# Optimization experiments

Measured on AMD Instinct MI355X. Metric: run time of the kernel, lower is better.

## Reference

```python
import jax, jax.numpy as jnp
import numpy as np

HEADS = 4


def setup_inputs() -> dict:
    key = jax.random.key(0)
    ks = jax.random.split(key, 6)
    b, c, d, h, w = 4, 512, 16, 16, 16
    x = jax.random.normal(ks[0], (b, c, d, h, w), dtype=jnp.float32)
    s = 0.02  # param init scale
    Wq = jax.random.normal(ks[1], (c, c), dtype=jnp.float32) * s
    Wk = jax.random.normal(ks[2], (c, c), dtype=jnp.float32) * s
    Wv = jax.random.normal(ks[3], (c, c), dtype=jnp.float32) * s
    Wproj = jax.random.normal(ks[4], (c, c), dtype=jnp.float32) * s
    bproj = jnp.zeros((c,), dtype=jnp.float32)
    return {"x": x, "Wq": Wq, "Wk": Wk, "Wv": Wv, "Wproj": Wproj, "bproj": bproj}


def reference(x, Wq, Wk, Wv, Wproj, bproj):
    b, c, d, h, w = x.shape
    N = d * h * w
    scale = (c // HEADS) ** -0.5  # module uses ch//heads for scale
    xf = x.reshape(b, c, N)  # (b, c, N)
    # 1x1 Conv1d == channel matmul
    q = jnp.einsum('oc,bcn->bon', Wq, xf)
    k = jnp.einsum('oc,bcn->bon', Wk, xf)
    v = jnp.einsum('oc,bcn->bon', Wv, xf)
    # Faithful to original (buggy) view: split SEQUENCE dim by heads -> (b, H, c, N//H)
    q = q.reshape(b, HEADS, c, N // HEADS)
    k = k.reshape(b, HEADS, c, N // HEADS)
    v = v.reshape(b, HEADS, c, N // HEADS)
    attn = jax.nn.softmax(jnp.einsum('bhqe,bhke->bhqk', q, k) * scale, axis=-1)
    out = jnp.einsum('bhqk,bhke->bhqe', attn, v)  # (b, H, c, N//H)
    out = jnp.swapaxes(out, 2, 3).reshape(b, c, N)  # matches transpose(2,3).view
    out = jnp.einsum('oc,bcn->bon', Wproj, out) + bproj[None, :, None]
    return out.reshape(b, c, d, h, w) + x
```

## Files before the change

### kernel.cpp

```cpp
#include <hip/hip_runtime.h>
#include <stdint.h>


typedef __attribute__((ext_vector_type(8))) short short8;
typedef __attribute__((ext_vector_type(4))) float f32x4;

typedef const __attribute__((address_space(1))) unsigned int* gas_ptr;
typedef __attribute__((address_space(3))) unsigned int* las_ptr;

#define ATTN_SCALE 0.08838834764831845f

__device__ __forceinline__ unsigned short f2bf(float f) {
    union { float f; unsigned int u; } c; c.f = f;
    unsigned int u = c.u;
    u += 0x7fffu + ((u >> 16) & 1u);
    return (unsigned short)(u >> 16);
}

__device__ __forceinline__ void gl_lds16(const void* g, void* l) {
    __builtin_amdgcn_global_load_lds((gas_ptr)(uintptr_t)g, (las_ptr)(uintptr_t)l,
                                     16, 0, 0);
}

template<int LDA, int LDB, int KDIM, bool PERMB = false>
__device__ __forceinline__ void mfma_core(
    const unsigned short* __restrict__ A,
    const unsigned short* __restrict__ B,
    int m0, int n0,
    unsigned short* __restrict__ sA, unsigned short* __restrict__ sB,
    f32x4 acc[4][4])
{
    const int tid  = threadIdx.x;
    const int lane = tid & 63, wave = tid >> 6;
    const int lr = lane >> 2, lc = lane & 3;
    const int wm = (wave & 1) * 64, wn = (wave >> 1) * 64;
    const int col = lane & 15, quad = lane >> 4;

    const unsigned short* ga = A + (size_t)(m0 + 32 * wave + lr) * LDA + lc * 8;
    int rb0 = n0 + 32 * wave + lr;
    int rb1 = rb0 + 16;
    if (PERMB) {
        rb0 = 4 * (rb0 & 127) + (rb0 >> 7);
        rb1 = 4 * (rb1 & 127) + (rb1 >> 7);
    }
    const unsigned short* gb0 = B + (size_t)rb0 * LDB + lc * 8;
    const unsigned short* gb1 = B + (size_t)rb1 * LDB + lc * 8;

    unsigned short* la0 = sA + (32 * wave) * 32;
    unsigned short* la1 = sA + (32 * wave + 16) * 32;
    unsigned short* lb0 = sB + (32 * wave) * 32;
    unsigned short* lb1 = sB + (32 * wave + 16) * 32;

    for (int k0 = 0; k0 < KDIM; k0 += 32) {
        gl_lds16(ga + k0,            la0);
        gl_lds16(ga + k0 + 16 * LDA, la1);
        gl_lds16(gb0 + k0,           lb0);
        gl_lds16(gb1 + k0,           lb1);
        __syncthreads();
        short8 af[4], bf[4];
        #pragma unroll
        for (int i = 0; i < 4; ++i)
            af[i] = *(const short8*)&sA[(wm + i * 16 + col) * 32 + quad * 8];
        #pragma unroll
        for (int j = 0; j < 4; ++j)
            bf[j] = *(const short8*)&sB[(wn + j * 16 + col) * 32 + quad * 8];
        #pragma unroll
        for (int i = 0; i < 4; ++i)
            #pragma unroll
            for (int j = 0; j < 4; ++j)
                acc[i][j] = __builtin_amdgcn_mfma_f32_16x16x32_bf16(
                    af[i], bf[j], acc[i][j], 0, 0, 0);
        __syncthreads();
    }
}

__global__ __launch_bounds__(256)
void prep(const float* __restrict__ x,
          const float* __restrict__ Wq, const float* __restrict__ Wk,
          const float* __restrict__ Wv, const float* __restrict__ Wp,
          unsigned short* __restrict__ xT, unsigned short* __restrict__ Wb)
{
    if (blockIdx.z == 4) {
        const int idx = (blockIdx.y * 64 + blockIdx.x) * 256 + threadIdx.x;
        const int mat = idx >> 16;
        const int off = (idx & 65535) << 2;
        const float* src = (mat == 0 ? Wq : mat == 1 ? Wk : mat == 2 ? Wv : Wp) + off;
        const float4 f = *(const float4*)src;
        uint2 o;
        o.x = f2bf(f.x) | ((unsigned)f2bf(f.y) << 16);
        o.y = f2bf(f.z) | ((unsigned)f2bf(f.w) << 16);
        *(uint2*)&Wb[mat * 262144 + off] = o;
        return;
    }
    const int b = blockIdx.z;
    const int l = threadIdx.x & 63, w = threadIdx.x >> 6;
    const int n  = blockIdx.x * 64 + l;
    const int c0 = blockIdx.y * 32 + w * 8;
    const float* xp = x + (size_t)b * 2097152 + (size_t)c0 * 4096 + n;
    unsigned int p[4];
    #pragma unroll
    for (int j = 0; j < 4; ++j) {
        const unsigned short a  = f2bf(xp[(2 * j)     * 4096]);
        const unsigned short bb = f2bf(xp[(2 * j + 1) * 4096]);
        p[j] = a | ((unsigned)bb << 16);
    }
    uint4 v; v.x = p[0]; v.y = p[1]; v.z = p[2]; v.w = p[3];
    *(uint4*)&xT[(size_t)b * 2097152 + (size_t)n * 512 + c0] = v;
}

__global__ __launch_bounds__(256)
void gemm_qkv(const unsigned short* __restrict__ Wb,
              const unsigned short* __restrict__ xT,
              unsigned short* __restrict__ qb, unsigned short* __restrict__ kb,
              unsigned short* __restrict__ vT)
{
    __shared__ unsigned short sA[128 * 32], sB[128 * 32];

    const int z = blockIdx.z, wsel = z >> 2, b = z & 3;
    const unsigned short* A = Wb + wsel * 262144;
    const unsigned short* B = xT + (size_t)b * 2097152;
    const int m0 = blockIdx.y * 128, n0 = blockIdx.x * 128;

    f32x4 z4 = {0.f, 0.f, 0.f, 0.f};
    f32x4 acc[4][4];
    #pragma unroll
    for (int i = 0; i < 4; ++i)
        #pragma unroll
        for (int j = 0; j < 4; ++j) acc[i][j] = z4;

    mfma_core<512, 512, 512>(A, B, m0, n0, sA, sB, acc);

    const int lane = threadIdx.x & 63, wave = threadIdx.x >> 6;
    const int wm = (wave & 1) * 64, wn = (wave >> 1) * 64;
    const int col = lane & 15, quad = lane >> 4;

    if (wsel < 2) {
        unsigned short* C = (wsel == 0 ? qb : kb) + (size_t)b * 2097152;
        #pragma unroll
        for (int i = 0; i < 4; ++i)
            #pragma unroll
            for (int r = 0; r < 4; ++r) {
                const int row = m0 + wm + i * 16 + quad * 4 + r;
                #pragma unroll
                for (int j = 0; j < 4; ++j)
                    C[(size_t)row * 4096 + n0 + wn + j * 16 + col] = f2bf(acc[i][j][r]);
            }
    } else {
        const int h = m0 >> 7, s = n0 >> 10, e0 = n0 & 1023;
        unsigned short* dst = vT + (size_t)(b * 4 + h) * 524288 + s * 128;
        #pragma unroll
        for (int i = 0; i < 4; ++i) {
            const int kb2 = wm + i * 16 + quad * 4;
            #pragma unroll
            for (int j = 0; j < 4; ++j) {
                const int e = e0 + wn + j * 16 + col;
                uint2 o;
                o.x = f2bf(acc[i][j][0]) | ((unsigned)f2bf(acc[i][j][1]) << 16);
                o.y = f2bf(acc[i][j][2]) | ((unsigned)f2bf(acc[i][j][3]) << 16);
                *(uint2*)&dst[(size_t)e * 512 + kb2] = o;
            }
        }
    }
}

__global__ __launch_bounds__(256)
void gemm_qk(const unsigned short* __restrict__ qb,
             const unsigned short* __restrict__ kb,
             float* __restrict__ S)
{
    __shared__ unsigned short sA[128 * 32], sB[128 * 32];
    const int z = blockIdx.z;
    const int slab = z >> 1, half = z & 1;
    const unsigned short* A = qb + (size_t)slab * 524288 + half * 512;
    const unsigned short* B = kb + (size_t)slab * 524288 + half * 512;
    float* Sp = S + (size_t)half * 4194304 + (size_t)slab * 262144;
    const int m0 = blockIdx.y * 128, n0 = blockIdx.x * 128;

    f32x4 z4 = {0.f, 0.f, 0.f, 0.f};
    f32x4 acc[4][4];
    #pragma unroll
    for (int i = 0; i < 4; ++i)
        #pragma unroll
        for (int j = 0; j < 4; ++j) acc[i][j] = z4;

    mfma_core<1024, 1024, 512, true>(A, B, m0, n0, sA, sB, acc);

    const int lane = threadIdx.x & 63, wave = threadIdx.x >> 6;
    const int wm = (wave & 1) * 64, wn = (wave >> 1) * 64;
    const int col = lane & 15, quad = lane >> 4;
    #pragma unroll
    for (int i = 0; i < 4; ++i)
        #pragma unroll
        for (int r = 0; r < 4; ++r) {
            const int row = m0 + wm + i * 16 + quad * 4 + r;
            #pragma unroll
            for (int j = 0; j < 4; ++j)
                Sp[(size_t)row * 512 + n0 + wn + j * 16 + col] =
                    acc[i][j][r] * ATTN_SCALE;
        }
}

__global__ __launch_bounds__(256)
void softmax_rows(const float* __restrict__ S, unsigned short* __restrict__ P)
{
    const int wave = threadIdx.x >> 6, lane = threadIdx.x & 63;
    const int row  = blockIdx.x * 4 + wave;
    const float* p0 = S + (size_t)row * 512;
    const float* p1 = p0 + 4194304;
    unsigned short* o = P + (size_t)row * 512;

    float vals[8];
    float m = -1e30f;
    #pragma unroll
    for (int t = 0; t < 8; ++t) {
        vals[t] = p0[lane + t * 64] + p1[lane + t * 64];
        m = fmaxf(m, vals[t]);
    }
    #pragma unroll
    for (int s = 32; s > 0; s >>= 1) m = fmaxf(m, __shfl_xor(m, s));
    float sum = 0.f;
    #pragma unroll
    for (int t = 0; t < 8; ++t) { vals[t] = __expf(vals[t] - m); sum += vals[t]; }
    #pragma unroll
    for (int s = 32; s > 0; s >>= 1) sum += __shfl_xor(sum, s);
    const float inv = 1.f / sum;
    #pragma unroll
    for (int t = 0; t < 8; ++t) o[lane + t * 64] = f2bf(vals[t] * inv);
}

__global__ __launch_bounds__(256)
void gemm_pv(const unsigned short* __restrict__ Pb,
             const unsigned short* __restrict__ vT,
             unsigned short* __restrict__ yT)
{
    __shared__ unsigned short sT[128 * 136];
    unsigned short* sA = sT;
    unsigned short* sB = sT + 4096;
    const int z = blockIdx.z, b = z >> 2, hh = z & 3;
    const unsigned short* A = Pb + (size_t)z * 262144;
    const unsigned short* B = vT + (size_t)z * 524288;
    unsigned short* yTb = yT + (size_t)b * 2097152;
    const int m0 = blockIdx.y * 128;
    const int n0 = blockIdx.x * 128;

    f32x4 z4 = {0.f, 0.f, 0.f, 0.f};
    f32x4 acc[4][4];
    #pragma unroll
    for (int i = 0; i < 4; ++i)
        #pragma unroll
        for (int j = 0; j < 4; ++j) acc[i][j] = z4;

    mfma_core<512, 512, 512>(A, B, m0, n0, sA, sB, acc);

    const int tid = threadIdx.x;
    const int lane = tid & 63, wave = tid >> 6;
    const int wm = (wave & 1) * 64, wn = (wave >> 1) * 64;
    const int col = lane & 15, quad = lane >> 4;

    #pragma unroll
    for (int i = 0; i < 4; ++i)
        #pragma unroll
        for (int r = 0; r < 4; ++r) {
            const int rr = wm + i * 16 + quad * 4 + r;
            #pragma unroll
            for (int j = 0; j < 4; ++j)
                sT[rr * 136 + wn + j * 16 + col] = f2bf(acc[i][j][r]);
        }
    __syncthreads();

    #pragma unroll
    for (int k = 0; k < 4; ++k) {
        const int rid = k * 256 + tid;
        const int qq_l = rid >> 3, s = rid & 7;
        const unsigned short* Trow = sT + qq_l * 136;
        unsigned int p[8];
        #pragma unroll
        for (int t = 0; t < 8; ++t) {
            const unsigned int a  = Trow[s + 8 * (2 * t)];
            const unsigned int bb = Trow[s + 8 * (2 * t + 1)];
            p[t] = a | (bb << 16);
        }
        const size_t base = (size_t)((s << 9) + m0 + qq_l) * 512 + hh * 128 + (n0 >> 3);
        uint4 lo; lo.x = p[0]; lo.y = p[1]; lo.z = p[2]; lo.w = p[3];
        uint4 hi; hi.x = p[4]; hi.y = p[5]; hi.z = p[6]; hi.w = p[7];
        *(uint4*)&yTb[base]     = lo;
        *(uint4*)&yTb[base + 8] = hi;
    }
}

__global__ __launch_bounds__(256)
void gemm_proj(const unsigned short* __restrict__ Wpb,
               const unsigned short* __restrict__ yT,
               const float* __restrict__ bias, const float* __restrict__ x,
               float* __restrict__ out)
{
    __shared__ unsigned short sA[128 * 32], sB[128 * 32];
    const int b = blockIdx.z;
    const unsigned short* B = yT + (size_t)b * 2097152;
    const int m0 = blockIdx.y * 128, n0 = blockIdx.x * 128;

    f32x4 z4 = {0.f, 0.f, 0.f, 0.f};
    f32x4 acc[4][4];
    #pragma unroll
    for (int i = 0; i < 4; ++i)
        #pragma unroll
        for (int j = 0; j < 4; ++j) acc[i][j] = z4;

    mfma_core<512, 512, 512>(Wpb, B, m0, n0, sA, sB, acc);

    const int lane = threadIdx.x & 63, wave = threadIdx.x >> 6;
    const int wm = (wave & 1) * 64, wn = (wave >> 1) * 64;
    const int col = lane & 15, quad = lane >> 4;
    const size_t boff = (size_t)b * 2097152;
    #pragma unroll
    for (int i = 0; i < 4; ++i)
        #pragma unroll
        for (int r = 0; r < 4; ++r) {
            const int row = m0 + wm + i * 16 + quad * 4 + r;
            const float bi = bias[row];
            #pragma unroll
            for (int j = 0; j < 4; ++j) {
                const size_t idx = boff + (size_t)row * 4096 + n0 + wn + j * 16 + col;
                out[idx] = acc[i][j][r] + bi + x[idx];
            }
        }
}

extern "C" void kernel_launch(void* const* d_in, const int* in_sizes, int n_in,
                              void* d_out, int out_size, void* d_ws, size_t ws_size,
                              hipStream_t stream) {
    const float* x     = (const float*)d_in[0];
    const float* Wq    = (const float*)d_in[1];
    const float* Wk    = (const float*)d_in[2];
    const float* Wv    = (const float*)d_in[3];
    const float* Wproj = (const float*)d_in[4];
    const float* bproj = (const float*)d_in[5];
    float* out = (float*)d_out;

    char* w = (char*)d_ws;
    unsigned short* xT = (unsigned short*)(w + 0);
    unsigned short* qb = (unsigned short*)(w + 16777216);
    unsigned short* kb = (unsigned short*)(w + 33554432);
    unsigned short* vT = (unsigned short*)(w + 50331648);
    float*          S  = (float*)        (w + 67108864);
    unsigned short* Pb = (unsigned short*)(w + 100663296);
    unsigned short* Wb = (unsigned short*)(w + 109051904);
    unsigned short* yT = xT;

    prep        <<<dim3(64, 16, 5),  256, 0, stream>>>(x, Wq, Wk, Wv, Wproj, xT, Wb);
    gemm_qkv    <<<dim3(32, 4, 12),  256, 0, stream>>>(Wb, xT, qb, kb, vT);
    gemm_qk     <<<dim3(4, 4, 32),   256, 0, stream>>>(qb, kb, S);
    softmax_rows<<<dim3(2048),       256, 0, stream>>>(S, Pb);
    gemm_pv     <<<dim3(8, 4, 16),   256, 0, stream>>>(Pb, vT, yT);
    gemm_proj   <<<dim3(32, 4, 4),   256, 0, stream>>>(Wb + 3 * 262144, yT, bproj, x, out);
}
```

Measured before the change: 206.1 us.

## Double-buffer LDS tiles in shared MFMA GEMM core and swizzle LDS layout

```diff
diff --git a/kernel.cpp b/kernel.cpp
--- a/kernel.cpp
+++ b/kernel.cpp
@@ -33,44 +33,65 @@
     const int tid  = threadIdx.x;
     const int lane = tid & 63, wave = tid >> 6;
     const int lr = lane >> 2, lc = lane & 3;
-    const int wm = (wave & 1) * 64, wn = (wave >> 1) * 64;
-    const int col = lane & 15, quad = lane >> 4;
-
-    const unsigned short* ga = A + (size_t)(m0 + 32 * wave + lr) * LDA + lc * 8;
+    const int lcs = lc ^ ((lr >> 1) & 3);
+    const int wm = (wave & 1) * 64, wn = (wave >> 1) * 64;
+    const int col = lane & 15, quad = lane >> 4;
+    const int swz = (quad ^ ((col >> 1) & 3)) * 8;
+
+    const unsigned short* ga = A + (size_t)(m0 + 32 * wave + lr) * LDA + lcs * 8;
     int rb0 = n0 + 32 * wave + lr;
     int rb1 = rb0 + 16;
     if (PERMB) {
         rb0 = 4 * (rb0 & 127) + (rb0 >> 7);
         rb1 = 4 * (rb1 & 127) + (rb1 >> 7);
     }
-    const unsigned short* gb0 = B + (size_t)rb0 * LDB + lc * 8;
-    const unsigned short* gb1 = B + (size_t)rb1 * LDB + lc * 8;
-
-    unsigned short* la0 = sA + (32 * wave) * 32;
-    unsigned short* la1 = sA + (32 * wave + 16) * 32;
-    unsigned short* lb0 = sB + (32 * wave) * 32;
-    unsigned short* lb1 = sB + (32 * wave + 16) * 32;
-
-    for (int k0 = 0; k0 < KDIM; k0 += 32) {
-        gl_lds16(ga + k0,            la0);
-        gl_lds16(ga + k0 + 16 * LDA, la1);
-        gl_lds16(gb0 + k0,           lb0);
-        gl_lds16(gb1 + k0,           lb1);
-        __syncthreads();
-        short8 af[4], bf[4];
+    const unsigned short* gb0 = B + (size_t)rb0 * LDB + lcs * 8;
+    const unsigned short* gb1 = B + (size_t)rb1 * LDB + lcs * 8;
+
+    const int wr0 = (32 * wave) * 32;
+    const int wr1 = (32 * wave + 16) * 32;
+
+    gl_lds16(ga,            sA + wr0);
+    gl_lds16(ga + 16 * LDA, sA + wr1);
+    gl_lds16(gb0,           sB + wr0);
+    gl_lds16(gb1,           sB + wr1);
+
+    constexpr int NK = KDIM / 32;
+    for (int kk = 0; kk < NK; ++kk) {
+        const int bo = (kk & 1) * 4096;
+        if (kk + 1 < NK) {
+            const int nb = ((kk + 1) & 1) * 4096;
+            const int k0 = (kk + 1) * 32;
+            gl_lds16(ga + k0,            sA + nb + wr0);
+            gl_lds16(ga + k0 + 16 * LDA, sA + nb + wr1);
+            gl_lds16(gb0 + k0,           sB + nb + wr0);
+            gl_lds16(gb1 + k0,           sB + nb + wr1);
+            asm volatile("s_waitcnt vmcnt(4)" ::: "memory");
+        } else {
+            asm volatile("s_waitcnt vmcnt(0)" ::: "memory");
+        }
+        __builtin_amdgcn_s_barrier();
+        asm volatile("" ::: "memory");
+        __builtin_amdgcn_sched_barrier(0);
+
+        const unsigned short* bA = sA + bo;
+        const unsigned short* bB = sB + bo;
+        short8 af[4], bfv[4];
         #pragma unroll
         for (int i = 0; i < 4; ++i)
-            af[i] = *(const short8*)&sA[(wm + i * 16 + col) * 32 + quad * 8];
+            af[i] = *(const short8*)&bA[(wm + i * 16 + col) * 32 + swz];
         #pragma unroll
         for (int j = 0; j < 4; ++j)
-            bf[j] = *(const short8*)&sB[(wn + j * 16 + col) * 32 + quad * 8];
+            bfv[j] = *(const short8*)&bB[(wn + j * 16 + col) * 32 + swz];
         #pragma unroll
         for (int i = 0; i < 4; ++i)
             #pragma unroll
             for (int j = 0; j < 4; ++j)
                 acc[i][j] = __builtin_amdgcn_mfma_f32_16x16x32_bf16(
-                    af[i], bf[j], acc[i][j], 0, 0, 0);
-        __syncthreads();
+                    af[i], bfv[j], acc[i][j], 0, 0, 0);
+
+        __builtin_amdgcn_s_barrier();
+        asm volatile("" ::: "memory");
     }
 }
 
@@ -114,7 +135,7 @@
               unsigned short* __restrict__ qb, unsigned short* __restrict__ kb,
               unsigned short* __restrict__ vT)
 {
-    __shared__ unsigned short sA[128 * 32], sB[128 * 32];
+    __shared__ unsigned short sA[2 * 128 * 32], sB[2 * 128 * 32];
 
     const int z = blockIdx.z, wsel = z >> 2, b = z & 3;
     const unsigned short* A = Wb + wsel * 262144;
@@ -168,7 +189,7 @@
              const unsigned short* __restrict__ kb,
              float* __restrict__ S)
 {
-    __shared__ unsigned short sA[128 * 32], sB[128 * 32];
+    __shared__ unsigned short sA[2 * 128 * 32], sB[2 * 128 * 32];
     const int z = blockIdx.z;
     const int slab = z >> 1, half = z & 1;
     const unsigned short* A = qb + (size_t)slab * 524288 + half * 512;
@@ -235,7 +256,7 @@
 {
     __shared__ unsigned short sT[128 * 136];
     unsigned short* sA = sT;
-    unsigned short* sB = sT + 4096;
+    unsigned short* sB = sT + 8192;
     const int z = blockIdx.z, b = z >> 2, hh = z & 3;
     const unsigned short* A = Pb + (size_t)z * 262144;
     const unsigned short* B = vT + (size_t)z * 524288;
@@ -252,6 +273,8 @@
 
     mfma_core<512, 512, 512>(A, B, m0, n0, sA, sB, acc);
 
+    __syncthreads();
+
     const int tid = threadIdx.x;
     const int lane = tid & 63, wave = tid >> 6;
     const int wm = (wave & 1) * 64, wn = (wave >> 1) * 64;
@@ -294,7 +317,7 @@
                const float* __restrict__ bias, const float* __restrict__ x,
                float* __restrict__ out)
 {
-    __shared__ unsigned short sA[128 * 32], sB[128 * 32];
+    __shared__ unsigned short sA[2 * 128 * 32], sB[2 * 128 * 32];
     const int b = blockIdx.z;
     const unsigned short* B = yT + (size_t)b * 2097152;
     const int m0 = blockIdx.y * 128, n0 = blockIdx.x * 128;
```

Result: faster. 199.0 us (-3.5%).
